# Performance work log

Hardware: AMD Instinct MI355X
Metric: run time of the kernel (lower is better)

Reference implementation:

```python
import jax, jax.numpy as jnp
import numpy as np

SCALES = (16, 32, 64, 128)
P = 8
D = 1024
H = 16
DEPTH = 8
MLP = 4096
NCLS = 1000
PB = [(s // P) ** 2 for s in SCALES]            # [4, 16, 64, 256]
BLOCKS = [PB[0] + 1] + PB[1:]                    # [5, 16, 64, 256]
L = sum(BLOCKS)                                  # 341
PATCH_L = sum(PB)                                # 340
PD = P * P * 3                                   # 192
HD = D // H
EPS = 1e-6

# scale id per token (start token belongs to scale 0)
_SID = np.concatenate([np.full(n, k, dtype=np.int32) for k, n in enumerate(BLOCKS)])
# additive block-causal mask: token in scale q may attend to scales <= q
_ALLOW = _SID[None, :] <= _SID[:, None]
MASK = jnp.where(jnp.asarray(_ALLOW), 0.0, -1e30).astype(jnp.float32)  # [L, L]
SID = jnp.asarray(_SID)


def _ln(x):
    m = jnp.mean(x, axis=-1, keepdims=True)
    v = jnp.var(x, axis=-1, keepdims=True)
    return (x - m) / jnp.sqrt(v + EPS)


def _l2n(t):
    n = jnp.sqrt(jnp.sum(t * t, axis=-1, keepdims=True))
    return t / jnp.maximum(n, 1e-12)


def setup_inputs() -> dict:
    key = jax.random.key(0)
    ks = jax.random.split(key, 16)
    s = 0.02
    inp = {
        "patches": jax.random.normal(ks[0], (8, PATCH_L, PD), jnp.float32),
        "labels": jax.random.randint(ks[1], (8,), 0, NCLS),
        "W_patch": s * jax.random.normal(ks[2], (PD, D), jnp.float32),
        "b_patch": jnp.zeros((D,), jnp.float32),
        "pos": s * jax.random.normal(ks[3], (1, L, D), jnp.float32),
        "scale_emb": s * jax.random.normal(ks[4], (len(SCALES), D), jnp.float32),
        "class_emb": s * jax.random.normal(ks[5], (NCLS + 1, D), jnp.float32),
        "ada_W": s * jax.random.normal(ks[6], (DEPTH, D, 6 * D), jnp.float32),
        "ada_b": jnp.zeros((DEPTH, 6 * D), jnp.float32),
        "qkv_W": s * jax.random.normal(ks[7], (DEPTH, D, 3 * D), jnp.float32),
        "qkv_b": jnp.zeros((DEPTH, 3 * D), jnp.float32),
        "q_scale": jnp.zeros((DEPTH, 1, 1, H, 1), jnp.float32),  # log-scale per head
        "proj_W": s * jax.random.normal(ks[8], (DEPTH, D, D), jnp.float32),
        "proj_b": jnp.zeros((DEPTH, D), jnp.float32),
        "fc1_W": s * jax.random.normal(ks[9], (DEPTH, D, MLP), jnp.float32),
        "fc1_b": jnp.zeros((DEPTH, MLP), jnp.float32),
        "fc2_W": s * jax.random.normal(ks[10], (DEPTH, MLP, D), jnp.float32),
        "fc2_b": jnp.zeros((DEPTH, D), jnp.float32),
        "head_ada_W": s * jax.random.normal(ks[11], (D, 2 * D), jnp.float32),
        "head_ada_b": jnp.zeros((2 * D,), jnp.float32),
        "head_W": s * jax.random.normal(ks[12], (D, PD), jnp.float32),
        "head_b": jnp.zeros((PD,), jnp.float32),
    }
    return inp


def reference(patches, labels, W_patch, b_patch, pos, scale_emb, class_emb,
              ada_W, ada_b, qkv_W, qkv_b, q_scale, proj_W, proj_b,
              fc1_W, fc1_b, fc2_W, fc2_b, head_ada_W, head_ada_b, head_W, head_b):
    B = patches.shape[0]
    cond = class_emb[labels]                              # [B, D]
    tok = patches @ W_patch + b_patch                     # [B, PATCH_L, D]
    x = jnp.concatenate([cond[:, None, :], tok], axis=1)  # [B, L, D]
    x = x + pos + scale_emb[SID]

    for i in range(DEPTH):
        ada = jax.nn.silu(cond) @ ada_W[i] + ada_b[i]     # [B, 6D]
        g1, g2, s1, s2, sh1, sh2 = [a[:, None, :] for a in jnp.split(ada, 6, axis=-1)]
        # attention branch
        h = _ln(x) * (s1 + 1.0) + sh1
        qkv = (h @ qkv_W[i] + qkv_b[i]).reshape(B, L, 3, H, HD)
        q, k, v = qkv[:, :, 0], qkv[:, :, 1], qkv[:, :, 2]  # [B, L, H, HD]
        q = _l2n(q) * jnp.exp(q_scale[i])                  # attn_l2_norm
        k = _l2n(k)
        scores = jnp.einsum("bqhd,bkhd->bhqk", q, k) + MASK
        attn = jax.nn.softmax(scores, axis=-1)
        o = jnp.einsum("bhqk,bkhd->bqhd", attn, v).reshape(B, L, D)
        x = x + g1 * (o @ proj_W[i] + proj_b[i])
        # mlp branch
        h2 = _ln(x) * (s2 + 1.0) + sh2
        m = jax.nn.gelu(h2 @ fc1_W[i] + fc1_b[i]) @ fc2_W[i] + fc2_b[i]
        x = x + g2 * m

    ada = jax.nn.silu(cond) @ head_ada_W + head_ada_b     # [B, 2D]
    sc, sh = [a[:, None, :] for a in jnp.split(ada, 2, axis=-1)]
    x = _ln(x) * (sc + 1.0) + sh
    return x @ head_W + head_b                            # [B, L, PD]
```

## Files before the change

kernel.cpp:

```cpp
#include <hip/hip_runtime.h>

typedef unsigned short ushort_t;
typedef __bf16 bf16x8 __attribute__((ext_vector_type(8)));
typedef float f32x4 __attribute__((ext_vector_type(4)));

#define DEV __device__ __forceinline__

DEV ushort_t f2bf(float x) {
  union { float f; unsigned u; } v; v.f = x;
  unsigned r = v.u + 0x7FFFu + ((v.u >> 16) & 1u);
  return (ushort_t)(r >> 16);
}
DEV int sid_of(int l) { return l < 5 ? 0 : (l < 21 ? 1 : (l < 85 ? 2 : 3)); }
DEV float fast_tanh(float u) { return 1.0f - 2.0f / (__expf(2.0f * u) + 1.0f); }
DEV float gelu_f(float x) {
  float u = 0.7978845608028654f * (x + 0.044715f * x * x * x);
  return 0.5f * x * (1.0f + fast_tanh(u));
}
DEV float silu_f(float x) { return x / (1.0f + __expf(-x)); }
DEV f32x4 mfma16(bf16x8 a, bf16x8 b, f32x4 c) {
  return __builtin_amdgcn_mfma_f32_16x16x32_bf16(a, b, c, 0, 0, 0);
}
DEV void gload16(const void* src, void* dst) {
  __builtin_amdgcn_global_load_lds(
      (const __attribute__((address_space(1))) void*)(uintptr_t)src,
      (__attribute__((address_space(3))) void*)(uintptr_t)dst, 16, 0, 0);
}

__global__ __launch_bounds__(256) void k_cond_x0(
    const int* __restrict__ labels, const float* __restrict__ class_emb,
    const float* __restrict__ pos, const float* __restrict__ semb,
    float* __restrict__ cond, float* __restrict__ x) {
  int b = blockIdx.x, t = threadIdx.x;
  int lab = labels[b];
  float4 cv = *(const float4*)&class_emb[(size_t)lab * 1024 + t * 4];
  *(float4*)&cond[(size_t)b * 1024 + t * 4] = cv;
  float4 pv = *(const float4*)&pos[t * 4];
  float4 sv = *(const float4*)&semb[t * 4];
  float4 xv;
  xv.x = cv.x + pv.x + sv.x; xv.y = cv.y + pv.y + sv.y;
  xv.z = cv.z + pv.z + sv.z; xv.w = cv.w + pv.w + sv.w;
  *(float4*)&x[(size_t)b * 341 * 1024 + t * 4] = xv;
}

__global__ __launch_bounds__(256) void k_convert(const float* __restrict__ src,
                                                 ushort_t* __restrict__ dst, int n4) {
  int i = blockIdx.x * 256 + threadIdx.x;
  if (i < n4) {
    float4 v = *(const float4*)&src[(size_t)i * 4];
    uint2 pk;
    pk.x = (unsigned)f2bf(v.x) | ((unsigned)f2bf(v.y) << 16);
    pk.y = (unsigned)f2bf(v.z) | ((unsigned)f2bf(v.w) << 16);
    *(uint2*)&dst[(size_t)i * 4] = pk;
  }
}

__global__ __launch_bounds__(256) void k_transpose(const float* __restrict__ src,
                                                   ushort_t* __restrict__ dst, int K, int N) {
  __shared__ ushort_t tile[32][33];
  int z = blockIdx.z;
  src += (size_t)z * K * N;
  dst += (size_t)z * K * N;
  int k0 = blockIdx.y * 32, n0 = blockIdx.x * 32;
  int t = threadIdx.x;
  int r = t >> 3, c = (t & 7) * 4;
  float4 v = *(const float4*)&src[(size_t)(k0 + r) * N + n0 + c];
  tile[r][c] = f2bf(v.x); tile[r][c + 1] = f2bf(v.y);
  tile[r][c + 2] = f2bf(v.z); tile[r][c + 3] = f2bf(v.w);
  __syncthreads();
  ushort_t o0 = tile[c][r], o1 = tile[c + 1][r], o2 = tile[c + 2][r], o3 = tile[c + 3][r];
  uint2 pk;
  pk.x = (unsigned)o0 | ((unsigned)o1 << 16);
  pk.y = (unsigned)o2 | ((unsigned)o3 << 16);
  *(uint2*)&dst[(size_t)(n0 + r) * K + k0 + c] = pk;
}

__global__ __launch_bounds__(256) void k_ada(const float* __restrict__ cond,
    const float* __restrict__ ada_W, const float* __restrict__ ada_b,
    const float* __restrict__ hada_W, const float* __restrict__ hada_b,
    float* __restrict__ ada_out, float* __restrict__ hada_out) {
  int gy = blockIdx.y;
  bool head = (gy == 8);
  int Nw = head ? 2048 : 6144;
  int n0 = blockIdx.x * 64;
  if (n0 >= Nw) return;
  __shared__ float sc[8 * 1024];
  __shared__ float red[4][64][8];
  int t = threadIdx.x;
  for (int i = t; i < 2048; i += 256) {
    float4 cv = *(const float4*)&cond[(size_t)i * 4];
    float* d = &sc[i * 4];
    d[0] = silu_f(cv.x); d[1] = silu_f(cv.y); d[2] = silu_f(cv.z); d[3] = silu_f(cv.w);
  }
  __syncthreads();
  const float* W = head ? hada_W : ada_W + (size_t)gy * 1024 * 6144;
  const float* bs = head ? hada_b : ada_b + (size_t)gy * 6144;
  float* op = head ? hada_out : ada_out + (size_t)gy * 8 * 6144;
  int col = n0 + (t & 63), kq = t >> 6;
  float acc[8] = {0.f, 0.f, 0.f, 0.f, 0.f, 0.f, 0.f, 0.f};
  for (int k = kq * 256; k < kq * 256 + 256; ++k) {
    float wv = W[(size_t)k * Nw + col];
#pragma unroll
    for (int b2 = 0; b2 < 8; ++b2) acc[b2] += wv * sc[b2 * 1024 + k];
  }
#pragma unroll
  for (int b2 = 0; b2 < 8; ++b2) red[kq][t & 63][b2] = acc[b2];
  __syncthreads();
  if (t < 64) {
    int colc = n0 + t;
    float bias = bs[colc];
#pragma unroll
    for (int b2 = 0; b2 < 8; ++b2) {
      float v = red[0][t][b2] + red[1][t][b2] + red[2][t][b2] + red[3][t][b2] + bias;
      op[(size_t)b2 * Nw + colc] = v;
    }
  }
}

__global__ __launch_bounds__(256) void k_ln(const float* __restrict__ x,
    ushort_t* __restrict__ hout, const float* __restrict__ ada,
    int stride, int soff, int shoff) {
  int row = blockIdx.x, t = threadIdx.x;
  int b = row / 341;
  const float* xr = x + (size_t)row * 1024;
  float4 xv = *(const float4*)&xr[t * 4];
  float s = xv.x + xv.y + xv.z + xv.w;
  float ss = xv.x * xv.x + xv.y * xv.y + xv.z * xv.z + xv.w * xv.w;
#pragma unroll
  for (int off = 1; off < 64; off <<= 1) { s += __shfl_xor(s, off); ss += __shfl_xor(ss, off); }
  __shared__ float red[8];
  int w = t >> 6, lane = t & 63;
  if (lane == 0) { red[w] = s; red[w + 4] = ss; }
  __syncthreads();
  s = red[0] + red[1] + red[2] + red[3];
  ss = red[4] + red[5] + red[6] + red[7];
  float mean = s * (1.f / 1024.f);
  float var = ss * (1.f / 1024.f) - mean * mean;
  float rstd = rsqrtf(var + 1e-6f);
  const float* ar = ada + (size_t)b * stride;
  float xe[4] = {xv.x, xv.y, xv.z, xv.w};
  ushort_t tmp[4];
#pragma unroll
  for (int j = 0; j < 4; ++j) {
    int n = t * 4 + j;
    float val = (xe[j] - mean) * rstd * (1.f + ar[soff + n]) + ar[shoff + n];
    tmp[j] = f2bf(val);
  }
  uint2 pk;
  pk.x = (unsigned)tmp[0] | ((unsigned)tmp[1] << 16);
  pk.y = (unsigned)tmp[2] | ((unsigned)tmp[3] << 16);
  *(uint2*)&hout[(size_t)row * 1024 + t * 4] = pk;
}

__global__ __launch_bounds__(256) void k_comb_ln(
    const float* __restrict__ p, const float* __restrict__ bias,
    const float* __restrict__ adag, int goff,
    float* __restrict__ x, const float* __restrict__ adaln,
    int lnstride, int soff, int shoff,
    ushort_t* __restrict__ hout, int nsplit) {
  int row = blockIdx.x, t = threadIdx.x;
  int b = row / 341;
  int c = t * 4;
  float4 s4 = *(const float4*)&p[(size_t)row * 1024 + c];
  if (nsplit == 2) {
    float4 q2 = *(const float4*)&p[(size_t)2728 * 1024 + (size_t)row * 1024 + c];
    s4.x += q2.x; s4.y += q2.y; s4.z += q2.z; s4.w += q2.w;
  }
  float4 bv = *(const float4*)&bias[c];
  const float* gr = adag + (size_t)b * 6144 + goff + c;
  float4 xv = *(float4*)&x[(size_t)row * 1024 + c];
  xv.x += gr[0] * (s4.x + bv.x);
  xv.y += gr[1] * (s4.y + bv.y);
  xv.z += gr[2] * (s4.z + bv.z);
  xv.w += gr[3] * (s4.w + bv.w);
  *(float4*)&x[(size_t)row * 1024 + c] = xv;
  float sm = xv.x + xv.y + xv.z + xv.w;
  float ss = xv.x * xv.x + xv.y * xv.y + xv.z * xv.z + xv.w * xv.w;
#pragma unroll
  for (int off = 1; off < 64; off <<= 1) { sm += __shfl_xor(sm, off); ss += __shfl_xor(ss, off); }
  __shared__ float red[8];
  int w = t >> 6, lane = t & 63;
  if (lane == 0) { red[w] = sm; red[w + 4] = ss; }
  __syncthreads();
  sm = red[0] + red[1] + red[2] + red[3];
  ss = red[4] + red[5] + red[6] + red[7];
  float mean = sm * (1.f / 1024.f);
  float var = ss * (1.f / 1024.f) - mean * mean;
  float rstd = rsqrtf(var + 1e-6f);
  const float* ar = adaln + (size_t)b * lnstride;
  float xe[4] = {xv.x, xv.y, xv.z, xv.w};
  ushort_t tmp[4];
#pragma unroll
  for (int j = 0; j < 4; ++j) {
    int n = c + j;
    float val = (xe[j] - mean) * rstd * (1.f + ar[soff + n]) + ar[shoff + n];
    tmp[j] = f2bf(val);
  }
  uint2 pk;
  pk.x = (unsigned)tmp[0] | ((unsigned)tmp[1] << 16);
  pk.y = (unsigned)tmp[2] | ((unsigned)tmp[3] << 16);
  *(uint2*)&hout[(size_t)row * 1024 + c] = pk;
}

template <int EPI, int BM>
__global__ __launch_bounds__(256, 3) void k_gemm(
    const ushort_t* __restrict__ A, const ushort_t* __restrict__ Bt,
    const float* __restrict__ bias, float* __restrict__ fout,
    ushort_t* __restrict__ bfout, const float* __restrict__ aux,
    float* __restrict__ xres, const float* __restrict__ pos,
    const float* __restrict__ semb, int M, int N, int K, int KS) {
  constexpr int NI = (BM == 128) ? 4 : 2;
  constexpr int WNB = (BM == 128) ? 64 : 32;
  __shared__ ushort_t aT[2][BM * 32];
  __shared__ ushort_t bT[2][128 * 32];
  int tid = threadIdx.x;
  int lane = tid & 63, w = tid >> 6;
  int WR = (BM == 128) ? (w >> 1) : 0;
  int WC = (BM == 128) ? (w & 1) : w;

  int gx = gridDim.x;
  int nwg = gx * gridDim.y;
  int orig = blockIdx.y * gx + blockIdx.x;
  int q = nwg >> 3, r8 = nwg & 7;
  int xcd = orig & 7, idx = orig >> 3;
  int lin = (xcd < r8 ? xcd * (q + 1) : r8 * (q + 1) + (xcd - r8) * q) + idx;
  int bx = lin % gx, by = lin / gx;

  int m0 = by * BM, n0 = bx * 128;
  int kbase = blockIdx.z * KS;
  f32x4 acc[4][NI];
#pragma unroll
  for (int i = 0; i < 4; ++i)
#pragma unroll
    for (int j = 0; j < NI; ++j) acc[i][j] = (f32x4){0.f, 0.f, 0.f, 0.f};

  int lrow = lane & 15;
  int csw = (lrow >> 1) & 3;
  int coff = ((lane >> 4) ^ csw) * 8;

  int s_row0 = tid >> 2, s_u = tid & 3;
  int s_c = s_u ^ ((s_row0 >> 1) & 3);
  int aR0 = m0 + s_row0; if (aR0 > M - 1) aR0 = M - 1;
  int bR0 = n0 + s_row0; if (bR0 > N - 1) bR0 = N - 1;
  int aR1 = m0 + s_row0 + 64; if (aR1 > M - 1) aR1 = M - 1;
  int bR1 = n0 + s_row0 + 64; if (bR1 > N - 1) bR1 = N - 1;
  const ushort_t* aSrc0 = A + (size_t)aR0 * K + kbase + s_c * 8;
  const ushort_t* aSrc1 = A + (size_t)aR1 * K + kbase + s_c * 8;
  const ushort_t* bSrc0 = Bt + (size_t)bR0 * K + kbase + s_c * 8;
  const ushort_t* bSrc1 = Bt + (size_t)bR1 * K + kbase + s_c * 8;
  int slot0 = w * 512, slot1 = 2048 + w * 512;

  int nsteps = KS >> 5;
  auto STAGE = [&](int k0, int buf) {
    gload16(aSrc0 + k0, &aT[buf][slot0]);
    if constexpr (BM == 128) gload16(aSrc1 + k0, &aT[buf][slot1]);
    gload16(bSrc0 + k0, &bT[buf][slot0]);
    gload16(bSrc1 + k0, &bT[buf][slot1]);
  };

  STAGE(0, 0);
  int cur = 0;
  for (int s = 0; s < nsteps; ++s) {
    int kn = (s + 1 < nsteps) ? ((s + 1) << 5) : 0;
    STAGE(kn, cur ^ 1);
    if constexpr (BM == 128)
      asm volatile("s_waitcnt vmcnt(4)" ::: "memory");
    else
      asm volatile("s_waitcnt vmcnt(3)" ::: "memory");
    __builtin_amdgcn_sched_barrier(0);
    __builtin_amdgcn_s_barrier();
    __builtin_amdgcn_sched_barrier(0);
    bf16x8 af[4], bb[NI];
#pragma unroll
    for (int mi = 0; mi < 4; ++mi)
      af[mi] = *(const bf16x8*)&aT[cur][(WR * 64 + mi * 16 + lrow) * 32 + coff];
#pragma unroll
    for (int ni = 0; ni < NI; ++ni)
      bb[ni] = *(const bf16x8*)&bT[cur][(WC * WNB + ni * 16 + lrow) * 32 + coff];
#pragma unroll
    for (int mi = 0; mi < 4; ++mi)
#pragma unroll
      for (int ni = 0; ni < NI; ++ni)
        acc[mi][ni] = mfma16(af[mi], bb[ni], acc[mi][ni]);
    __builtin_amdgcn_sched_barrier(0);
    __builtin_amdgcn_s_barrier();
    __builtin_amdgcn_sched_barrier(0);
    cur ^= 1;
  }

  if constexpr (EPI == 6) {
    int nb = n0 + WC * 64;
    int gh = nb >> 6;
    float qse = (gh < 16) ? __expf(aux[gh]) : 1.0f;
    bool dn = gh < 32;
#pragma unroll
    for (int mi = 0; mi < 4; ++mi) {
#pragma unroll
      for (int r = 0; r < 4; ++r) {
        float vv[4]; float ss = 0.f;
#pragma unroll
        for (int ni = 0; ni < 4; ++ni) {
          vv[ni] = acc[mi][ni][r] + bias[nb + ni * 16 + lrow];
          ss += vv[ni] * vv[ni];
        }
        if (dn) {
          ss += __shfl_xor(ss, 1); ss += __shfl_xor(ss, 2);
          ss += __shfl_xor(ss, 4); ss += __shfl_xor(ss, 8);
          float rn = qse / fmaxf(sqrtf(ss), 1e-12f);
#pragma unroll
          for (int ni = 0; ni < 4; ++ni) vv[ni] *= rn;
        }
        int gm = m0 + WR * 64 + mi * 16 + (lane >> 4) * 4 + r;
        if (gm < M) {
#pragma unroll
          for (int ni = 0; ni < 4; ++ni)
            bfout[(size_t)gm * N + nb + ni * 16 + lrow] = f2bf(vv[ni]);
        }
      }
    }
  } else {
#pragma unroll
    for (int mi = 0; mi < 4; ++mi) {
#pragma unroll
      for (int ni = 0; ni < NI; ++ni) {
#pragma unroll
        for (int r = 0; r < 4; ++r) {
          int gm = m0 + WR * 64 + mi * 16 + (lane >> 4) * 4 + r;
          int gn = n0 + WC * WNB + ni * 16 + lrow;
          if (gm >= M || gn >= N) continue;
          if constexpr (EPI == 7) {
            fout[(size_t)blockIdx.z * M * N + (size_t)gm * N + gn] = acc[mi][ni][r];
          } else {
            float v = acc[mi][ni][r] + bias[gn];
            if constexpr (EPI == 2) {
              bfout[(size_t)gm * N + gn] = f2bf(gelu_f(v));
            } else if constexpr (EPI == 4) {
              int b = gm / 340, l = gm % 340 + 1;
              float val = v + pos[(size_t)l * 1024 + gn] + semb[(size_t)sid_of(l) * 1024 + gn];
              xres[((size_t)(b * 341 + l)) * 1024 + gn] = val;
            }
          }
        }
      }
    }
  }
}

__global__ __launch_bounds__(256) void k_comb_head(const float* __restrict__ p,
    const float* __restrict__ bias, float* __restrict__ out, int nsplit) {
  int row = blockIdx.x, t = threadIdx.x;
  const int N = 192;
  size_t stride = (size_t)2728 * N;
  if (t < 48) {
    int c = t * 4;
    float4 s = *(const float4*)&p[(size_t)row * N + c];
    for (int sp = 1; sp < nsplit; ++sp) {
      float4 qq = *(const float4*)&p[sp * stride + (size_t)row * N + c];
      s.x += qq.x; s.y += qq.y; s.z += qq.z; s.w += qq.w;
    }
    float4 bv = *(const float4*)&bias[c];
    s.x += bv.x; s.y += bv.y; s.z += bv.z; s.w += bv.w;
    *(float4*)&out[(size_t)row * N + c] = s;
  }
}

__global__ __launch_bounds__(256) void k_attn(
    const ushort_t* __restrict__ qkv, ushort_t* __restrict__ o) {
  int qt = blockIdx.x, h = blockIdx.y, b = blockIdx.z;
  int t = threadIdx.x, lane = t & 63, w = t >> 6;
  int q0 = qt * 64;
  __shared__ ushort_t qT[64 * 72], kT[64 * 72], vS[64 * 72], vT[64 * 72];
  __shared__ ushort_t pT[4][16 * 72];
#pragma unroll
  for (int i = 0; i < 2; ++i) {
    int vid = t + 256 * i;
    int row = vid >> 3, seg = (vid & 7) * 8;
    int l = q0 + row; if (l > 340) l = 340;
    uint4 v = *(const uint4*)&qkv[((size_t)(b * 341 + l)) * 3072 + h * 64 + seg];
    *(uint4*)&qT[row * 72 + seg] = v;
  }
  int lrow = lane & 15, lk8 = (lane >> 4) * 8;
  int sq[4];
  float mrun[4], lsum[4];
  f32x4 accO[4];
#pragma unroll
  for (int r = 0; r < 4; ++r) {
    int lq = q0 + w * 16 + (lane >> 4) * 4 + r;
    sq[r] = sid_of(lq < 341 ? lq : 340);
    mrun[r] = -1e30f;
    lsum[r] = 0.f;
  }
#pragma unroll
  for (int d = 0; d < 4; ++d) accO[d] = (f32x4){0.f, 0.f, 0.f, 0.f};
  int nch = (qt == 0) ? 2 : 6;
  int vd = t >> 2, vlseg = (t & 3) * 16;

  uint4 kr[2], vr[2];
  auto ldkv = [&](int c) {
#pragma unroll
    for (int i = 0; i < 2; ++i) {
      int vid = t + 256 * i;
      int row = vid >> 3, seg = (vid & 7) * 8;
      int l = c * 64 + row; if (l > 340) l = 340;
      size_t base = ((size_t)(b * 341 + l)) * 3072 + h * 64 + seg;
      kr[i] = *(const uint4*)&qkv[base + 1024];
      vr[i] = *(const uint4*)&qkv[base + 2048];
    }
  };
  ldkv(0);
  for (int c = 0; c < nch; ++c) {
    __syncthreads();
#pragma unroll
    for (int i = 0; i < 2; ++i) {
      int vid = t + 256 * i;
      int row = vid >> 3, seg = (vid & 7) * 8;
      *(uint4*)&kT[row * 72 + seg] = kr[i];
      *(uint4*)&vS[row * 72 + seg] = vr[i];
    }
    __syncthreads();
    if (c + 1 < nch) ldkv(c + 1);
    ushort_t tmp[16];
#pragma unroll
    for (int j = 0; j < 16; ++j) tmp[j] = vS[(vlseg + j) * 72 + vd];
    f32x4 sf[4];
#pragma unroll
    for (int nf = 0; nf < 4; ++nf) sf[nf] = (f32x4){0.f, 0.f, 0.f, 0.f};
    __builtin_amdgcn_s_setprio(1);
#pragma unroll
    for (int ks = 0; ks < 2; ++ks) {
      bf16x8 aq = *(const bf16x8*)&qT[(w * 16 + lrow) * 72 + ks * 32 + lk8];
#pragma unroll
      for (int nf = 0; nf < 4; ++nf) {
        bf16x8 bk = *(const bf16x8*)&kT[(nf * 16 + lrow) * 72 + ks * 32 + lk8];
        sf[nf] = mfma16(aq, bk, sf[nf]);
      }
    }
    __builtin_amdgcn_s_setprio(0);
#pragma unroll
    for (int nf = 0; nf < 4; ++nf) {
      int lk = c * 64 + nf * 16 + lrow;
      int sk = lk < 341 ? sid_of(lk) : 9;
#pragma unroll
      for (int r = 0; r < 4; ++r)
        if (sk > sq[r]) sf[nf][r] = -1e30f;
    }
    float rs[4];
#pragma unroll
    for (int r = 0; r < 4; ++r) {
      float m = sf[0][r];
      m = fmaxf(m, sf[1][r]); m = fmaxf(m, sf[2][r]); m = fmaxf(m, sf[3][r]);
#pragma unroll
      for (int off = 1; off < 16; off <<= 1) m = fmaxf(m, __shfl_xor(m, off));
      float mn = fmaxf(mrun[r], m);
      float scl = __expf(mrun[r] - mn);
      mrun[r] = mn;
      lsum[r] *= scl;
#pragma unroll
      for (int d = 0; d < 4; ++d) accO[d][r] *= scl;
      rs[r] = 0.f;
    }
    ushort_t* pw = &pT[w][0];
#pragma unroll
    for (int nf = 0; nf < 4; ++nf) {
#pragma unroll
      for (int r = 0; r < 4; ++r) {
        float p = __expf(sf[nf][r] - mrun[r]);
        rs[r] += p;
        pw[((lane >> 4) * 4 + r) * 72 + nf * 16 + lrow] = f2bf(p);
      }
    }
#pragma unroll
    for (int r = 0; r < 4; ++r) {
      float sum = rs[r];
#pragma unroll
      for (int off = 1; off < 16; off <<= 1) sum += __shfl_xor(sum, off);
      lsum[r] += sum;
    }
    {
      uint4 s0, s1;
      s0.x = (unsigned)tmp[0] | ((unsigned)tmp[1] << 16);
      s0.y = (unsigned)tmp[2] | ((unsigned)tmp[3] << 16);
      s0.z = (unsigned)tmp[4] | ((unsigned)tmp[5] << 16);
      s0.w = (unsigned)tmp[6] | ((unsigned)tmp[7] << 16);
      s1.x = (unsigned)tmp[8] | ((unsigned)tmp[9] << 16);
      s1.y = (unsigned)tmp[10] | ((unsigned)tmp[11] << 16);
      s1.z = (unsigned)tmp[12] | ((unsigned)tmp[13] << 16);
      s1.w = (unsigned)tmp[14] | ((unsigned)tmp[15] << 16);
      *(uint4*)&vT[vd * 72 + vlseg] = s0;
      *(uint4*)&vT[vd * 72 + vlseg + 8] = s1;
    }
    __syncthreads();
    __builtin_amdgcn_s_setprio(1);
#pragma unroll
    for (int ks = 0; ks < 2; ++ks) {
      bf16x8 ap = *(const bf16x8*)&pw[lrow * 72 + ks * 32 + lk8];
#pragma unroll
      for (int d = 0; d < 4; ++d) {
        bf16x8 bv = *(const bf16x8*)&vT[(d * 16 + lrow) * 72 + ks * 32 + lk8];
        accO[d] = mfma16(ap, bv, accO[d]);
      }
    }
    __builtin_amdgcn_s_setprio(0);
  }
#pragma unroll
  for (int d = 0; d < 4; ++d) {
#pragma unroll
    for (int r = 0; r < 4; ++r) {
      int lq = q0 + w * 16 + (lane >> 4) * 4 + r;
      if (lq < 341) {
        float ov = accO[d][r] / fmaxf(lsum[r], 1e-30f);
        o[((size_t)(b * 341 + lq)) * 1024 + h * 64 + d * 16 + lrow] = f2bf(ov);
      }
    }
  }
}

extern "C" void kernel_launch(void* const* d_in, const int* in_sizes, int n_in,
                              void* d_out, int out_size, void* d_ws, size_t ws_size,
                              hipStream_t stream) {
  const float* patches   = (const float*)d_in[0];
  const int*   labels    = (const int*)d_in[1];
  const float* W_patch   = (const float*)d_in[2];
  const float* b_patch   = (const float*)d_in[3];
  const float* pos       = (const float*)d_in[4];
  const float* scale_emb = (const float*)d_in[5];
  const float* class_emb = (const float*)d_in[6];
  const float* ada_W     = (const float*)d_in[7];
  const float* ada_b     = (const float*)d_in[8];
  const float* qkv_W     = (const float*)d_in[9];
  const float* qkv_b     = (const float*)d_in[10];
  const float* q_scale   = (const float*)d_in[11];
  const float* proj_W    = (const float*)d_in[12];
  const float* proj_b    = (const float*)d_in[13];
  const float* fc1_W     = (const float*)d_in[14];
  const float* fc1_b     = (const float*)d_in[15];
  const float* fc2_W     = (const float*)d_in[16];
  const float* fc2_b     = (const float*)d_in[17];
  const float* hada_W    = (const float*)d_in[18];
  const float* hada_b    = (const float*)d_in[19];
  const float* head_W    = (const float*)d_in[20];
  const float* head_b    = (const float*)d_in[21];
  (void)in_sizes; (void)n_in; (void)out_size; (void)ws_size;

  char* wsb = (char*)d_ws;
  size_t off = 0;
  auto alloc = [&](size_t bytes) -> void* {
    void* p = wsb + off;
    off = (off + bytes + 255) & ~(size_t)255;
    return p;
  };

  float*    f_cond   = (float*)alloc(8 * 1024 * 4);
  float*    f_ada    = (float*)alloc((size_t)8 * 8 * 6144 * 4);
  float*    f_hada   = (float*)alloc(8 * 2048 * 4);
  float*    f_x      = (float*)alloc((size_t)2728 * 1024 * 4);
  ushort_t* u_h      = (ushort_t*)alloc((size_t)2728 * 1024 * 2);
  ushort_t* u_qkv    = (ushort_t*)alloc((size_t)2728 * 3072 * 2);
  ushort_t* u_o      = (ushort_t*)alloc((size_t)2728 * 1024 * 2);
  ushort_t* u_mid    = (ushort_t*)alloc((size_t)2728 * 4096 * 2);
  float*    f_part   = (float*)alloc((size_t)2 * 2728 * 1024 * 4);
  ushort_t* u_patch  = (ushort_t*)alloc((size_t)2720 * 192 * 2);
  ushort_t* u_qkvt   = (ushort_t*)alloc((size_t)8 * 3072 * 1024 * 2);
  ushort_t* u_projt  = (ushort_t*)alloc((size_t)8 * 1024 * 1024 * 2);
  ushort_t* u_fc1t   = (ushort_t*)alloc((size_t)8 * 4096 * 1024 * 2);
  ushort_t* u_fc2t   = (ushort_t*)alloc((size_t)8 * 1024 * 4096 * 2);
  ushort_t* u_wpt    = (ushort_t*)alloc((size_t)1024 * 192 * 2);
  ushort_t* u_wht    = (ushort_t*)alloc((size_t)192 * 1024 * 2);

  const int MT = 22;
  const int MT64 = 43;

  k_cond_x0<<<8, 256, 0, stream>>>(labels, class_emb, pos, scale_emb, f_cond, f_x);
  k_transpose<<<dim3(32, 6, 1), 256, 0, stream>>>(W_patch, u_wpt, 192, 1024);
  k_transpose<<<dim3(6, 32, 1), 256, 0, stream>>>(head_W, u_wht, 1024, 192);
  k_convert<<<510, 256, 0, stream>>>(patches, u_patch, 130560);
  k_ada<<<dim3(96, 9), 256, 0, stream>>>(f_cond, ada_W, ada_b, hada_W, hada_b, f_ada, f_hada);
  k_transpose<<<dim3(96, 32, 8), 256, 0, stream>>>(qkv_W, u_qkvt, 1024, 3072);
  k_transpose<<<dim3(32, 32, 8), 256, 0, stream>>>(proj_W, u_projt, 1024, 1024);
  k_transpose<<<dim3(128, 32, 8), 256, 0, stream>>>(fc1_W, u_fc1t, 1024, 4096);
  k_transpose<<<dim3(32, 128, 8), 256, 0, stream>>>(fc2_W, u_fc2t, 4096, 1024);

  k_gemm<4, 128><<<dim3(8, MT), 256, 0, stream>>>(u_patch, u_wpt, b_patch, nullptr, nullptr,
                                                  nullptr, f_x, pos, scale_emb, 2720, 1024, 192, 192);
  k_ln<<<2728, 256, 0, stream>>>(f_x, u_h, f_ada, 6144, 2048, 4096);

  for (int i = 0; i < 8; ++i) {
    const float* adaL = f_ada + (size_t)i * 8 * 6144;
    k_gemm<6, 128><<<dim3(24, MT), 256, 0, stream>>>(u_h, u_qkvt + (size_t)i * 3072 * 1024,
                                                     qkv_b + (size_t)i * 3072, nullptr, u_qkv,
                                                     q_scale + (size_t)i * 16, nullptr, nullptr,
                                                     nullptr, 2728, 3072, 1024, 1024);
    k_attn<<<dim3(6, 16, 8), 256, 0, stream>>>(u_qkv, u_o);
    k_gemm<7, 64><<<dim3(8, MT64, 2), 256, 0, stream>>>(u_o, u_projt + (size_t)i * 1024 * 1024,
                                                        nullptr, f_part, nullptr, nullptr,
                                                        nullptr, nullptr, nullptr,
                                                        2728, 1024, 1024, 512);
    k_comb_ln<<<2728, 256, 0, stream>>>(f_part, proj_b + (size_t)i * 1024, adaL, 0,
                                        f_x, adaL, 6144, 3072, 5120, u_h, 2);
    k_gemm<2, 128><<<dim3(32, MT), 256, 0, stream>>>(u_h, u_fc1t + (size_t)i * 4096 * 1024,
                                                     fc1_b + (size_t)i * 4096, nullptr,
                                                     u_mid, nullptr, nullptr, nullptr, nullptr,
                                                     2728, 4096, 1024, 1024);
    k_gemm<7, 64><<<dim3(8, MT64, 2), 256, 0, stream>>>(u_mid, u_fc2t + (size_t)i * 4096 * 1024,
                                                        nullptr, f_part, nullptr, nullptr,
                                                        nullptr, nullptr, nullptr,
                                                        2728, 1024, 4096, 2048);
    if (i < 7) {
      k_comb_ln<<<2728, 256, 0, stream>>>(f_part, fc2_b + (size_t)i * 1024, adaL, 1024,
                                          f_x, f_ada + (size_t)(i + 1) * 8 * 6144,
                                          6144, 2048, 4096, u_h, 2);
    } else {
      k_comb_ln<<<2728, 256, 0, stream>>>(f_part, fc2_b + (size_t)i * 1024, adaL, 1024,
                                          f_x, f_hada, 2048, 0, 1024, u_h, 2);
    }
  }

  k_gemm<7, 64><<<dim3(2, MT64, 4), 256, 0, stream>>>(u_h, u_wht, nullptr, f_part, nullptr,
                                                      nullptr, nullptr, nullptr, nullptr,
                                                      2728, 192, 1024, 256);
  k_comb_head<<<2728, 256, 0, stream>>>(f_part, head_b, (float*)d_out, 4);
}
```

Baseline: 1.985 ms.

## Fuse proj bias/gate residual into GEMM epilogue, drop split-K, unpipeline attn KV loads

The attention output projection now runs as a single non-split GEMM whose epilogue adds bias, multiplies by the adaLN gate and accumulates straight into the fp32 residual. The following k_comb_ln is replaced by a plain k_ln. This removes the fp32 partial-sum buffer round trip and the split-K reduction, at the cost of fewer blocks (no z split) for a K=1024 GEMM. Separately, the attention kernel drops its register prefetch of the next K/V chunk and loads each chunk synchronously, which trades latency hiding for lower register pressure. k_comb_ln also loses its nsplit parameter and always sums two partials.

```diff
diff --git a/kernel.cpp b/kernel.cpp
--- a/kernel.cpp
+++ b/kernel.cpp
@@ -157,15 +157,13 @@
     const float* __restrict__ adag, int goff,
     float* __restrict__ x, const float* __restrict__ adaln,
     int lnstride, int soff, int shoff,
-    ushort_t* __restrict__ hout, int nsplit) {
+    ushort_t* __restrict__ hout) {
   int row = blockIdx.x, t = threadIdx.x;
   int b = row / 341;
   int c = t * 4;
   float4 s4 = *(const float4*)&p[(size_t)row * 1024 + c];
-  if (nsplit == 2) {
-    float4 q2 = *(const float4*)&p[(size_t)2728 * 1024 + (size_t)row * 1024 + c];
-    s4.x += q2.x; s4.y += q2.y; s4.z += q2.z; s4.w += q2.w;
-  }
+  float4 q2 = *(const float4*)&p[(size_t)2728 * 1024 + (size_t)row * 1024 + c];
+  s4.x += q2.x; s4.y += q2.y; s4.z += q2.z; s4.w += q2.w;
   float4 bv = *(const float4*)&bias[c];
   const float* gr = adag + (size_t)b * 6144 + goff + c;
   float4 xv = *(float4*)&x[(size_t)row * 1024 + c];
@@ -332,7 +330,10 @@
             fout[(size_t)blockIdx.z * M * N + (size_t)gm * N + gn] = acc[mi][ni][r];
           } else {
             float v = acc[mi][ni][r] + bias[gn];
-            if constexpr (EPI == 2) {
+            if constexpr (EPI == 1) {
+              int b = gm / 341;
+              xres[(size_t)gm * 1024 + gn] += aux[(size_t)b * 6144 + gn] * v;
+            } else if constexpr (EPI == 2) {
               bfout[(size_t)gm * N + gn] = f2bf(gelu_f(v));
             } else if constexpr (EPI == 4) {
               int b = gm / 340, l = gm % 340 + 1;
@@ -394,31 +395,20 @@
   for (int d = 0; d < 4; ++d) accO[d] = (f32x4){0.f, 0.f, 0.f, 0.f};
   int nch = (qt == 0) ? 2 : 6;
   int vd = t >> 2, vlseg = (t & 3) * 16;
-
-  uint4 kr[2], vr[2];
-  auto ldkv = [&](int c) {
+  for (int c = 0; c < nch; ++c) {
+    __syncthreads();
 #pragma unroll
     for (int i = 0; i < 2; ++i) {
       int vid = t + 256 * i;
       int row = vid >> 3, seg = (vid & 7) * 8;
       int l = c * 64 + row; if (l > 340) l = 340;
       size_t base = ((size_t)(b * 341 + l)) * 3072 + h * 64 + seg;
-      kr[i] = *(const uint4*)&qkv[base + 1024];
-      vr[i] = *(const uint4*)&qkv[base + 2048];
-    }
-  };
-  ldkv(0);
-  for (int c = 0; c < nch; ++c) {
+      uint4 kv = *(const uint4*)&qkv[base + 1024];
+      uint4 vv = *(const uint4*)&qkv[base + 2048];
+      *(uint4*)&kT[row * 72 + seg] = kv;
+      *(uint4*)&vS[row * 72 + seg] = vv;
+    }
     __syncthreads();
-#pragma unroll
-    for (int i = 0; i < 2; ++i) {
-      int vid = t + 256 * i;
-      int row = vid >> 3, seg = (vid & 7) * 8;
-      *(uint4*)&kT[row * 72 + seg] = kr[i];
-      *(uint4*)&vS[row * 72 + seg] = vr[i];
-    }
-    __syncthreads();
-    if (c + 1 < nch) ldkv(c + 1);
     ushort_t tmp[16];
 #pragma unroll
     for (int j = 0; j < 16; ++j) tmp[j] = vS[(vlseg + j) * 72 + vd];
@@ -591,12 +581,11 @@
                                                      q_scale + (size_t)i * 16, nullptr, nullptr,
                                                      nullptr, 2728, 3072, 1024, 1024);
     k_attn<<<dim3(6, 16, 8), 256, 0, stream>>>(u_qkv, u_o);
-    k_gemm<7, 64><<<dim3(8, MT64, 2), 256, 0, stream>>>(u_o, u_projt + (size_t)i * 1024 * 1024,
-                                                        nullptr, f_part, nullptr, nullptr,
-                                                        nullptr, nullptr, nullptr,
-                                                        2728, 1024, 1024, 512);
-    k_comb_ln<<<2728, 256, 0, stream>>>(f_part, proj_b + (size_t)i * 1024, adaL, 0,
-                                        f_x, adaL, 6144, 3072, 5120, u_h, 2);
+    k_gemm<1, 64><<<dim3(8, MT64, 1), 256, 0, stream>>>(u_o, u_projt + (size_t)i * 1024 * 1024,
+                                                        proj_b + (size_t)i * 1024, nullptr,
+                                                        nullptr, adaL, f_x, nullptr, nullptr,
+                                                        2728, 1024, 1024, 1024);
+    k_ln<<<2728, 256, 0, stream>>>(f_x, u_h, adaL, 6144, 3072, 5120);
     k_gemm<2, 128><<<dim3(32, MT), 256, 0, stream>>>(u_h, u_fc1t + (size_t)i * 4096 * 1024,
                                                      fc1_b + (size_t)i * 4096, nullptr,
                                                      u_mid, nullptr, nullptr, nullptr, nullptr,
@@ -608,10 +597,10 @@
     if (i < 7) {
       k_comb_ln<<<2728, 256, 0, stream>>>(f_part, fc2_b + (size_t)i * 1024, adaL, 1024,
                                           f_x, f_ada + (size_t)(i + 1) * 8 * 6144,
-                                          6144, 2048, 4096, u_h, 2);
+                                          6144, 2048, 4096, u_h);
     } else {
       k_comb_ln<<<2728, 256, 0, stream>>>(f_part, fc2_b + (size_t)i * 1024, adaL, 1024,
-                                          f_x, f_hada, 2048, 0, 1024, u_h, 2);
+                                          f_x, f_hada, 2048, 0, 1024, u_h);
     }
   }
 
```

Measured after the change: 1.780 ms. 10.3% less time.
